# Kernel optimization log

Measured on AMD Instinct MI355X. Metric: run time of the kernel, lower is better.

The kernel has to match this reference:

```python
import jax, jax.numpy as jnp
import numpy as np

TOPK = 300
IMG_SZ = 1280.0
B, N, C = 128, 33600, 6


def setup_inputs() -> dict:
    key = jax.random.key(0)
    preds = jax.random.normal(key, (B, N, C), dtype=jnp.float32)
    return {"preds": preds}


def reference(preds):
    # preds: [B, N, 6] = (x1_abs, y1_abs, x2_abs, y2_abs, conf, cls)
    scores = preds[:, :, 4]                                   # [B, N]
    # top-k over anchor dim, largest, sorted descending (matches torch.topk)
    topk_scores, topk_idx = jax.lax.top_k(scores, TOPK)       # [B, K]
    # gather the full 6-dim rows of the selected anchors
    sel = jnp.take_along_axis(preds, topk_idx[:, :, None], axis=1)  # [B, K, 6]
    inv = jnp.float32(1.0 / IMG_SZ)
    x1 = sel[:, :, 0] * inv
    y1 = sel[:, :, 1] * inv
    x2 = sel[:, :, 2] * inv
    y2 = sel[:, :, 3] * inv
    conf = sel[:, :, 4]
    cls = sel[:, :, 5]
    w = x2 - x1
    h = y2 - y1
    cx = (x1 + x2) * jnp.float32(0.5)
    cy = (y1 + y2) * jnp.float32(0.5)
    return jnp.stack([cx, cy, w, h, conf, cls], axis=2)       # [B, K, 6]
```

## Files before the change

### kernel.cpp

```cpp
#include <hip/hip_runtime.h>
#include <stdint.h>

#define BATCH 128
#define NELEM 33600
#define NCH 6
#define TOPK 300
#define NTHREADS 1024
#define PER_THREAD 33
#define CAP 768

__device__ __forceinline__ uint32_t fkey(float f) {
    uint32_t u = __float_as_uint(f);
    return (u & 0x80000000u) ? ~u : (u | 0x80000000u);
}

__global__ __launch_bounds__(NTHREADS) void yolo_post_topk(
    const float* __restrict__ preds, float* __restrict__ out)
{
    const int b   = blockIdx.x;
    const int tid = threadIdx.x;
    const int wave = tid >> 6;
    const float* row = preds + (size_t)b * (NELEM * NCH);

    __shared__ uint32_t hist[256][16];
    __shared__ uint32_t suf[257];
    __shared__ uint32_t h2[257];
    __shared__ uint64_t cand[CAP];
    __shared__ uint32_t ccount;
    __shared__ uint32_t sh_b1, sh_S1, sh_thr;

    for (int i = tid; i < 256 * 16; i += NTHREADS) ((uint32_t*)hist)[i] = 0;
    if (tid == 0) ccount = 0;
    __syncthreads();

    uint32_t key[PER_THREAD];
    #pragma unroll
    for (int j = 0; j < PER_THREAD; ++j) {
        int i = tid + j * NTHREADS;
        if (i < NELEM) {
            float s = row[(size_t)i * NCH + 4];
            uint32_t k = fkey(s);
            key[j] = k;
            atomicAdd(&hist[k >> 24][wave], 1u);
        } else {
            key[j] = 0u;
        }
    }
    __syncthreads();

    if (tid < 256) {
        uint32_t s = 0;
        #pragma unroll
        for (int w = 0; w < 16; ++w) s += hist[tid][w];
        suf[tid] = s;
        if (tid == 0) suf[256] = 0;
    }
    __syncthreads();

    for (int d = 1; d < 256; d <<= 1) {
        uint32_t t = 0;
        if (tid < 256 && tid + d < 256) t = suf[tid + d];
        __syncthreads();
        if (tid < 256) suf[tid] += t;
        __syncthreads();
    }
    if (tid < 256) {
        uint32_t hi = (tid == 255) ? 0u : suf[tid + 1];
        if (suf[tid] >= TOPK && hi < TOPK) { sh_b1 = (uint32_t)tid; sh_S1 = hi; }
    }
    if (tid < 257) h2[tid] = 0;
    __syncthreads();
    const uint32_t b1 = sh_b1, S1 = sh_S1;

    #pragma unroll
    for (int j = 0; j < PER_THREAD; ++j) {
        int i = tid + j * NTHREADS;
        if (i < NELEM && (key[j] >> 24) == b1)
            atomicAdd(&h2[(key[j] >> 16) & 0xFFu], 1u);
    }
    __syncthreads();
    for (int d = 1; d < 256; d <<= 1) {
        uint32_t t = 0;
        if (tid < 256 && tid + d < 256) t = h2[tid + d];
        __syncthreads();
        if (tid < 256) h2[tid] += t;
        __syncthreads();
    }
    if (tid < 256) {
        uint32_t hi = (tid == 255) ? 0u : h2[tid + 1];
        if (S1 + h2[tid] >= TOPK && S1 + hi < TOPK)
            sh_thr = (b1 << 8) | (uint32_t)tid;
    }
    __syncthreads();
    const uint32_t thr = sh_thr;

    #pragma unroll
    for (int j = 0; j < PER_THREAD; ++j) {
        int i = tid + j * NTHREADS;
        if (i < NELEM && (key[j] >> 16) >= thr) {
            uint32_t pos = atomicAdd(&ccount, 1u);
            if (pos < CAP)
                cand[pos] = ((uint64_t)key[j] << 32) | (uint32_t)(~(uint32_t)i);
        }
    }
    __syncthreads();
    const int Cn = (int)min(ccount, (uint32_t)CAP);

    if (tid < Cn) {
        const uint64_t mine = cand[tid];
        int rank = 0;
        for (int j = 0; j < Cn; ++j) rank += (cand[j] > mine) ? 1 : 0;
        if (rank < TOPK) {
            uint32_t idx = ~(uint32_t)(mine & 0xFFFFFFFFu);
            const float* e = row + (size_t)idx * NCH;
            float p0 = e[0], p1 = e[1], p2 = e[2], p3 = e[3], p4 = e[4], p5 = e[5];
            const float inv = 1.0f / 1280.0f;
            float x1 = p0 * inv, y1 = p1 * inv, x2 = p2 * inv, y2 = p3 * inv;
            float* o = out + (size_t)b * (TOPK * NCH) + (size_t)rank * NCH;
            o[0] = (x1 + x2) * 0.5f;
            o[1] = (y1 + y2) * 0.5f;
            o[2] = x2 - x1;
            o[3] = y2 - y1;
            o[4] = p4;
            o[5] = p5;
        }
    }
}

extern "C" void kernel_launch(void* const* d_in, const int* in_sizes, int n_in,
                              void* d_out, int out_size, void* d_ws, size_t ws_size,
                              hipStream_t stream) {
    const float* preds = (const float*)d_in[0];
    float* out = (float*)d_out;
    hipLaunchKernelGGL(yolo_post_topk, dim3(BATCH), dim3(NTHREADS), 0, stream,
                       preds, out);
}
```

Before: 31.03 us.

## Split each batch row across two blocks with a separate merge-and-rank kernel

Each batch row is now split into two halves, each handled by its own block. A block computes a per-half top-300 candidate set through a two-level radix histogram and writes it to workspace. A second kernel merges the two candidate lists per row, ranks them and gathers the outputs. This doubles the block count to fill more compute units and halves per-thread register keys. In exchange it adds a second launch, a global-memory round trip and a larger candidate set to rank. The histogram layout is also transposed to wave-major.

```diff
diff --git a/kernel.cpp b/kernel.cpp
--- a/kernel.cpp
+++ b/kernel.cpp
@@ -3,57 +3,58 @@
 
 #define BATCH 128
 #define NELEM 33600
-#define NCH 6
-#define TOPK 300
-#define NTHREADS 1024
-#define PER_THREAD 33
-#define CAP 768
+#define HALF  16800
+#define NCH   6
+#define TOPK  300
+#define NT1   1024
+#define PT    17
+#define CAP2  448
+#define NT2   1024
 
 __device__ __forceinline__ uint32_t fkey(float f) {
     uint32_t u = __float_as_uint(f);
     return (u & 0x80000000u) ? ~u : (u | 0x80000000u);
 }
 
-__global__ __launch_bounds__(NTHREADS) void yolo_post_topk(
-    const float* __restrict__ preds, float* __restrict__ out)
+__global__ __launch_bounds__(NT1) void k1_select(
+    const float* __restrict__ preds, uint64_t* __restrict__ cand_g,
+    uint32_t* __restrict__ cnt_g)
 {
-    const int b   = blockIdx.x;
-    const int tid = threadIdx.x;
+    const int blk  = blockIdx.x;
+    const int b    = blk >> 1;
+    const int seg  = blk & 1;
+    const int tid  = threadIdx.x;
     const int wave = tid >> 6;
     const float* row = preds + (size_t)b * (NELEM * NCH);
+    const int base_i = seg * HALF;
 
-    __shared__ uint32_t hist[256][16];
-    __shared__ uint32_t suf[257];
-    __shared__ uint32_t h2[257];
-    __shared__ uint64_t cand[CAP];
-    __shared__ uint32_t ccount;
-    __shared__ uint32_t sh_b1, sh_S1, sh_thr;
+    __shared__ uint32_t hist[16][256];
+    __shared__ uint32_t suf[256];
+    __shared__ uint32_t h2[256];
+    __shared__ uint32_t sh_b1, sh_S1, sh_thr, ccount;
 
-    for (int i = tid; i < 256 * 16; i += NTHREADS) ((uint32_t*)hist)[i] = 0;
+    for (int i = tid; i < 16 * 256; i += NT1) ((uint32_t*)hist)[i] = 0;
     if (tid == 0) ccount = 0;
     __syncthreads();
 
-    uint32_t key[PER_THREAD];
+    uint32_t key[PT];
     #pragma unroll
-    for (int j = 0; j < PER_THREAD; ++j) {
-        int i = tid + j * NTHREADS;
-        if (i < NELEM) {
-            float s = row[(size_t)i * NCH + 4];
+    for (int j = 0; j < PT; ++j) {
+        int li = tid + j * NT1;
+        if (li < HALF) {
+            float s = row[(size_t)(base_i + li) * NCH + 4];
             uint32_t k = fkey(s);
             key[j] = k;
-            atomicAdd(&hist[k >> 24][wave], 1u);
-        } else {
-            key[j] = 0u;
-        }
+            atomicAdd(&hist[wave][k >> 24], 1u);
+        } else key[j] = 0u;
     }
     __syncthreads();
 
     if (tid < 256) {
         uint32_t s = 0;
         #pragma unroll
-        for (int w = 0; w < 16; ++w) s += hist[tid][w];
+        for (int w = 0; w < 16; ++w) s += hist[w][tid];
         suf[tid] = s;
-        if (tid == 0) suf[256] = 0;
     }
     __syncthreads();
 
@@ -67,15 +68,15 @@
     if (tid < 256) {
         uint32_t hi = (tid == 255) ? 0u : suf[tid + 1];
         if (suf[tid] >= TOPK && hi < TOPK) { sh_b1 = (uint32_t)tid; sh_S1 = hi; }
+        h2[tid] = 0;
     }
-    if (tid < 257) h2[tid] = 0;
     __syncthreads();
     const uint32_t b1 = sh_b1, S1 = sh_S1;
 
     #pragma unroll
-    for (int j = 0; j < PER_THREAD; ++j) {
-        int i = tid + j * NTHREADS;
-        if (i < NELEM && (key[j] >> 24) == b1)
+    for (int j = 0; j < PT; ++j) {
+        int li = tid + j * NT1;
+        if (li < HALF && (key[j] >> 24) == b1)
             atomicAdd(&h2[(key[j] >> 16) & 0xFFu], 1u);
     }
     __syncthreads();
@@ -94,17 +95,39 @@
     __syncthreads();
     const uint32_t thr = sh_thr;
 
+    uint64_t* cbase = cand_g + (size_t)blk * CAP2;
     #pragma unroll
-    for (int j = 0; j < PER_THREAD; ++j) {
-        int i = tid + j * NTHREADS;
-        if (i < NELEM && (key[j] >> 16) >= thr) {
+    for (int j = 0; j < PT; ++j) {
+        int li = tid + j * NT1;
+        if (li < HALF && (key[j] >> 16) >= thr) {
             uint32_t pos = atomicAdd(&ccount, 1u);
-            if (pos < CAP)
-                cand[pos] = ((uint64_t)key[j] << 32) | (uint32_t)(~(uint32_t)i);
+            if (pos < CAP2)
+                cbase[pos] = ((uint64_t)key[j] << 32)
+                           | (uint32_t)(~(uint32_t)(base_i + li));
         }
     }
     __syncthreads();
-    const int Cn = (int)min(ccount, (uint32_t)CAP);
+    if (tid == 0) cnt_g[blk] = min(ccount, (uint32_t)CAP2);
+}
+
+__global__ __launch_bounds__(NT2) void k2_rank(
+    const float* __restrict__ preds, const uint64_t* __restrict__ cand_g,
+    const uint32_t* __restrict__ cnt_g, float* __restrict__ out)
+{
+    const int b   = blockIdx.x;
+    const int tid = threadIdx.x;
+
+    __shared__ uint64_t cand[2 * CAP2];
+    __shared__ uint32_t c0s, c1s;
+
+    if (tid == 0) { c0s = cnt_g[2 * b]; c1s = cnt_g[2 * b + 1]; }
+    __syncthreads();
+    const int c0 = (int)c0s, c1 = (int)c1s;
+    const int Cn = c0 + c1;
+
+    if (tid < c0)            cand[tid] = cand_g[(size_t)(2 * b) * CAP2 + tid];
+    else if (tid - c0 < c1)  cand[tid] = cand_g[(size_t)(2 * b + 1) * CAP2 + (tid - c0)];
+    __syncthreads();
 
     if (tid < Cn) {
         const uint64_t mine = cand[tid];
@@ -112,7 +135,7 @@
         for (int j = 0; j < Cn; ++j) rank += (cand[j] > mine) ? 1 : 0;
         if (rank < TOPK) {
             uint32_t idx = ~(uint32_t)(mine & 0xFFFFFFFFu);
-            const float* e = row + (size_t)idx * NCH;
+            const float* e = preds + (size_t)b * (NELEM * NCH) + (size_t)idx * NCH;
             float p0 = e[0], p1 = e[1], p2 = e[2], p3 = e[3], p4 = e[4], p5 = e[5];
             const float inv = 1.0f / 1280.0f;
             float x1 = p0 * inv, y1 = p1 * inv, x2 = p2 * inv, y2 = p3 * inv;
@@ -132,6 +155,12 @@
                               hipStream_t stream) {
     const float* preds = (const float*)d_in[0];
     float* out = (float*)d_out;
-    hipLaunchKernelGGL(yolo_post_topk, dim3(BATCH), dim3(NTHREADS), 0, stream,
-                       preds, out);
+
+    uint64_t* cand_g = (uint64_t*)d_ws;
+    uint32_t* cnt_g  = (uint32_t*)((char*)d_ws + (size_t)2 * BATCH * CAP2 * sizeof(uint64_t));
+
+    hipLaunchKernelGGL(k1_select, dim3(2 * BATCH), dim3(NT1), 0, stream,
+                       preds, cand_g, cnt_g);
+    hipLaunchKernelGGL(k2_rank, dim3(BATCH), dim3(NT2), 0, stream,
+                       preds, cand_g, cnt_g, out);
 }
```

Result: slower. 40.86 us (+31.7%).
